# Optimization experiments

Measured on AMD Instinct MI355X. Metric: run time of the kernel, lower is better.

Reference implementation:

```python
import jax, jax.numpy as jnp
import numpy as np

B, D, H, W = 32, 64, 32, 32
M = 1024  # codebook_size


def setup_inputs() -> dict:
    key = jax.random.key(0)
    k1, k2, k3 = jax.random.split(key, 3)
    z = jax.random.normal(k1, (B, D, H, W), dtype=jnp.float32)
    codebook = jax.random.normal(k2, (M, D), dtype=jnp.float32)
    noise = jax.random.normal(k3, (B * H * W, D), dtype=jnp.float32)
    return {"z": z, "codebook": codebook, "noise": noise}


def reference(z, codebook, noise):
    b, d, h, w = z.shape
    n = b * h * w
    # (B,D,H,W) -> (B,H,W,D) -> (N,D)
    zf = jnp.transpose(z, (0, 2, 3, 1)).reshape(n, d)
    x2 = jnp.sum(zf * zf, axis=1, keepdims=True)          # (N,1)
    y2 = jnp.sum(codebook * codebook, axis=1)[None, :]    # (1,M)
    dist = x2 + y2 - 2.0 * (zf @ codebook.T)              # (N,M)
    dist_min = jnp.min(dist, axis=1, keepdims=True)       # (N,1)
    ind = jnp.argmin(dist, axis=1)                        # (N,) int
    # noise substitution: unit-norm random direction scaled by sqrt(min dist)
    nrm = jnp.maximum(jnp.linalg.norm(noise, axis=-1, keepdims=True), 1e-9)
    q_error = noise / nrm * jnp.sqrt(jnp.maximum(dist_min, 0.0))
    z_q = zf + q_error                                    # (N,D)
    # torch: z_q.view(B, D, H*W) is a raw memory reshape of the (B*H*W, D) buffer
    z_q_view = z_q.reshape(b, d, h * w)                   # (B,D,HW)
    # loss = mean over (B,HW,HW) of z_q_view^T @ z_q_view
    #      = sum_b sum_d (sum_n z_q_view[b,d,n])^2 / (B * HW^2)  (no HWxHW intermediate)
    s = jnp.sum(z_q_view, axis=2)                         # (B,D)
    hw = h * w
    loss = jnp.sum(s * s) / (b * hw * hw)
    z_q_out = jnp.transpose(z_q.reshape(b, h, w, d), (0, 3, 1, 2))  # (B,D,H,W)
    return z_q_out, loss, ind
```

## Files before the change

kernel.cpp:

```cpp
#include <hip/hip_runtime.h>
#include <hip/hip_bf16.h>

#define BB 32
#define DD 64
#define HW 1024
#define NN 32768
#define MM 1024

typedef _Float16 half8 __attribute__((ext_vector_type(8)));
typedef float    floatx4 __attribute__((ext_vector_type(4)));

#define MFMA16(a, b, c) __builtin_amdgcn_mfma_f32_16x16x32_f16((a), (b), (c), 0, 0, 0)

#define LO_SCALE   2048.0f
#define LO_INV     (1.0f / 2048.0f)

typedef __attribute__((address_space(1))) const void* gas_t;
typedef __attribute__((address_space(3)))       void* las_t;
#define ASYNC16(g, l) __builtin_amdgcn_global_load_lds((gas_t)(g), (las_t)(l), 16, 0, 0)

__global__ void k_prep(const float* __restrict__ cb,
                       _Float16* __restrict__ ch,
                       _Float16* __restrict__ cl,
                       float* __restrict__ y2,
                       float* __restrict__ loss_slot) {
    int u = blockIdx.x * blockDim.x + threadIdx.x;
    if (u == 0) *loss_slot = 0.0f;

    if (u < 64 * 2 * 64) {
        int lane  = u & 63;
        int kstep = (u >> 6) & 1;
        int mtile = u >> 7;
        int m  = mtile * 16 + (lane & 15);
        int d0 = kstep * 32 + ((lane >> 4) & 3) * 8;
        const float* src = cb + (size_t)m * DD + d0;
        half8 h, l;
#pragma unroll
        for (int j = 0; j < 8; ++j) {
            float x = -2.0f * src[j];
            _Float16 hi = (_Float16)x;
            _Float16 lo = (_Float16)((x - (float)hi) * LO_SCALE);
            h[j] = hi;
            l[j] = lo;
        }
        *(half8*)(ch + (size_t)u * 8) = h;
        *(half8*)(cl + (size_t)u * 8) = l;
    }

    if (u < MM) {
        const float4* c4 = (const float4*)(cb + (size_t)u * DD);
        float s = 0.f;
#pragma unroll
        for (int k = 0; k < 16; ++k) {
            float4 v = c4[k];
            s += v.x * v.x + v.y * v.y + v.z * v.z + v.w * v.w;
        }
        y2[u] = s;
    }
}

__global__ __launch_bounds__(512) void k_main(const float* __restrict__ z,
                                              const float* __restrict__ noise,
                                              const _Float16* __restrict__ ch,
                                              const _Float16* __restrict__ cl,
                                              const float* __restrict__ y2,
                                              float* __restrict__ zq,
                                              float* __restrict__ ind_out,
                                              float* __restrict__ loss_slot) {
    __shared__ float zt[64][65];
    __shared__ float y2s[MM];
    __shared__ float x2p[64][8];
    __shared__ float snorm[64];
    __shared__ float scale_s[64];
    __shared__ float bestv_s[4][64];
    __shared__ int   besti_s[4][64];
    __shared__ float partials[512];
    __shared__ float sq[4];
    __shared__ __align__(16) char ubuf[2 * 16384];

    half8* bufB8 = (half8*)ubuf;
    float (*nt)[65] = (float (*)[65])ubuf;

    const int t    = threadIdx.x;
    const int lane = t & 63;
    const int wv   = t >> 6;
    const int mi   = wv & 3;
    const int rh   = wv >> 2;
    const int quad = lane >> 4;
    const int col  = lane & 15;
    const int blk  = blockIdx.x;
    const int b    = blk >> 4;
    const int hw0  = (blk & 15) << 6;

    const half8* ch8 = (const half8*)ch;
    const half8* cl8 = (const half8*)cl;

    const half8* gseg = (wv < 4) ? (ch8 + wv * 128) : (cl8 + (wv - 4) * 128);
    half8* l0 = bufB8 + wv * 128;
    half8* l1 = bufB8 + 1024 + wv * 128;

    ASYNC16(gseg + lane,      l0);
    ASYNC16(gseg + 64 + lane, l0 + 64);

    const float* zbase = z + ((size_t)b << 16) + hw0;

    for (int i = t; i < 64 * 64; i += 512) {
        int d = i >> 6, r = i & 63;
        zt[r][d] = zbase[(size_t)d * HW + r];
    }
    for (int i = t; i < MM; i += 512) y2s[i] = y2[i];
    __syncthreads();

    {
        int row = t & 63, seg = t >> 6;
        float s = 0.f;
#pragma unroll
        for (int j = 0; j < 8; ++j) {
            float v = zt[row][seg * 8 + j];
            s = __builtin_fmaf(v, v, s);
        }
        x2p[row][seg] = s;
    }

    half8 ah[2][2], al[2][2];
#pragma unroll
    for (int n2 = 0; n2 < 2; ++n2) {
        int row = rh * 32 + n2 * 16 + col;
#pragma unroll
        for (int ks = 0; ks < 2; ++ks) {
            int d0 = ks * 32 + quad * 8;
            half8 h, l;
#pragma unroll
            for (int j = 0; j < 8; ++j) {
                float x = zt[row][d0 + j];
                _Float16 hi = (_Float16)x;
                _Float16 lo = (_Float16)((x - (float)hi) * LO_SCALE);
                h[j] = hi;
                l[j] = lo;
            }
            ah[n2][ks] = h;
            al[n2][ks] = l;
        }
    }

    float best[8];
    int   bmt[8];
#pragma unroll
    for (int s = 0; s < 8; ++s) { best[s] = 1e30f; bmt[s] = 0; }

#pragma unroll 2
    for (int c = 0; c < 16; ++c) {
        const int p = c & 1;
        if (c) __syncthreads();

        if (c < 15) {
            const half8* gs = gseg + (c + 1) * 512;
            half8* ls = ((c + 1) & 1) ? l1 : l0;
            ASYNC16(gs + lane,      ls);
            ASYNC16(gs + 64 + lane, ls + 64);
        }

        const half8* bp = bufB8 + p * 1024;
        half8 bh0 = bp[(mi * 2 + 0) * 64 + lane];
        half8 bh1 = bp[(mi * 2 + 1) * 64 + lane];
        half8 bl0 = bp[512 + (mi * 2 + 0) * 64 + lane];
        half8 bl1 = bp[512 + (mi * 2 + 1) * 64 + lane];

        const int mt = c * 4 + mi;
        float y2v = y2s[(mt << 4) + col];
        floatx4 a1[2], a2[2];
#pragma unroll
        for (int n2 = 0; n2 < 2; ++n2) {
            floatx4 i1 = {y2v, y2v, y2v, y2v};
            floatx4 i2 = {0.f, 0.f, 0.f, 0.f};
            a1[n2] = i1;
            a2[n2] = i2;
        }
#pragma unroll
        for (int n2 = 0; n2 < 2; ++n2) {
            a1[n2] = MFMA16(ah[n2][0], bh0, a1[n2]);
            a2[n2] = MFMA16(al[n2][0], bh0, a2[n2]);
            a2[n2] = MFMA16(ah[n2][0], bl0, a2[n2]);
            a1[n2] = MFMA16(ah[n2][1], bh1, a1[n2]);
            a2[n2] = MFMA16(al[n2][1], bh1, a2[n2]);
            a2[n2] = MFMA16(ah[n2][1], bl1, a2[n2]);
        }
#pragma unroll
        for (int n2 = 0; n2 < 2; ++n2) {
#pragma unroll
            for (int r = 0; r < 4; ++r) {
                float v = __builtin_fmaf(a2[n2][r], LO_INV, a1[n2][r]);
                int s = n2 * 4 + r;
                bool cc = v < best[s];
                best[s] = cc ? v : best[s];
                bmt[s]  = cc ? mt : bmt[s];
            }
        }
    }
    __syncthreads();

    {
        const float4* noise4 = (const float4*)noise;
        const size_t base4 = (size_t)blk * 1024;
#pragma unroll
        for (int k = 0; k < 2; ++k) {
            int v = t + 512 * k;
            float4 vv = noise4[base4 + v];
            int c  = v >> 4;
            int d0 = (v & 15) << 2;
            nt[d0 + 0][c] = vv.x;
            nt[d0 + 1][c] = vv.y;
            nt[d0 + 2][c] = vv.z;
            nt[d0 + 3][c] = vv.w;
            float p = vv.x * vv.x + vv.y * vv.y + vv.z * vv.z + vv.w * vv.w;
            p += __shfl_xor(p, 1);
            p += __shfl_xor(p, 2);
            p += __shfl_xor(p, 4);
            p += __shfl_xor(p, 8);
            if ((t & 15) == 0) snorm[c] = p;
        }
    }

#pragma unroll
    for (int n2 = 0; n2 < 2; ++n2) {
#pragma unroll
        for (int r = 0; r < 4; ++r) {
            int s = n2 * 4 + r;
            float v  = best[s];
            int  idx = bmt[s] * 16 + col;
#pragma unroll
            for (int mask = 1; mask <= 8; mask <<= 1) {
                float v2 = __shfl_xor(v, mask);
                int   i2 = __shfl_xor(idx, mask);
                if (v2 < v || (v2 == v && i2 < idx)) { v = v2; idx = i2; }
            }
            if (col == 0) {
                int rl = rh * 32 + n2 * 16 + quad * 4 + r;
                bestv_s[mi][rl] = v;
                besti_s[mi][rl] = idx;
            }
        }
    }
    __syncthreads();

    if (t < 64) {
        float bv = bestv_s[0][t];
        int   bi = besti_s[0][t];
#pragma unroll
        for (int w = 1; w < 4; ++w) {
            float v = bestv_s[w][t];
            int   ix = besti_s[w][t];
            if (v < bv || (v == bv && ix < bi)) { bv = v; bi = ix; }
        }
        float x2 = 0.f;
#pragma unroll
        for (int s = 0; s < 8; ++s) x2 += x2p[t][s];
        float dm = x2 + bv;
        int n = (blk << 6) + t;
        ind_out[n] = (float)bi;
        float nr = fmaxf(sqrtf(snorm[t]), 1e-9f);
        scale_s[t] = sqrtf(fmaxf(dm, 0.f)) / nr;
    }
    __syncthreads();

    float acc = 0.f;
    const size_t obase = ((size_t)b << 16) + hw0;
#pragma unroll
    for (int it = 0; it < 8; ++it) {
        int flat = it * 512 + t;
        int d = flat >> 6;
        int c = t & 63;
        float v = zt[c][d] + nt[d][c] * scale_s[c];
        zq[obase + (size_t)d * HW + c] = v;
        acc += v;
    }

    partials[t] = acc;
    __syncthreads();
    if (t < 4) {
        float s = 0.f;
        for (int g = 0; g < 8; ++g)
            for (int j = 0; j < 16; ++j)
                s += partials[g * 64 + t * 16 + j];
        sq[t] = s * s;
    }
    __syncthreads();
    if (t == 0) {
        float contrib = (sq[0] + sq[1] + sq[2] + sq[3]) * (1.0f / 33554432.0f);
        atomicAdd(loss_slot, contrib);
    }
}

extern "C" void kernel_launch(void* const* d_in, const int* in_sizes, int n_in,
                              void* d_out, int out_size, void* d_ws, size_t ws_size,
                              hipStream_t stream) {
    const float* z        = (const float*)d_in[0];
    const float* codebook = (const float*)d_in[1];
    const float* noise    = (const float*)d_in[2];

    float* out      = (float*)d_out;
    float* zq_out   = out;
    float* loss_ptr = out + 2097152;
    float* ind_out  = out + 2097153;

    float* y2       = (float*)d_ws;
    _Float16* ch    = (_Float16*)(y2 + MM);
    _Float16* cl    = ch + 65536;

    k_prep<<<16,  512, 0, stream>>>(codebook, ch, cl, y2, loss_ptr);
    k_main<<<512, 512, 0, stream>>>(z, noise, ch, cl, y2,
                                    zq_out, ind_out, loss_ptr);
}
```

Before: 99.95 us.

## Double rows per block to 128 and halve grid to reuse codebook tiles

Each block now handles 128 spatial rows instead of 64, with 8 waves arranged as 4 row groups by 2 codebook groups, each wave covering two 16-wide codebook tiles per chunk. This halves the number of blocks and so halves total codebook streaming through LDS per output row, amortizing the async codebook loads over more MFMA work. Noise staging, the reductions and the loss partials are resized to match. The trade-off is 256 blocks on a GPU with 256 CUs, so there is less parallelism to hide latency, plus higher LDS use per block.

```diff
diff --git a/kernel.cpp b/kernel.cpp
--- a/kernel.cpp
+++ b/kernel.cpp
@@ -67,30 +67,30 @@
                                               float* __restrict__ zq,
                                               float* __restrict__ ind_out,
                                               float* __restrict__ loss_slot) {
-    __shared__ float zt[64][65];
+    __shared__ float zt[128][65];
     __shared__ float y2s[MM];
-    __shared__ float x2p[64][8];
-    __shared__ float snorm[64];
-    __shared__ float scale_s[64];
-    __shared__ float bestv_s[4][64];
-    __shared__ int   besti_s[4][64];
+    __shared__ float x2p[128][4];
+    __shared__ float snorm[128];
+    __shared__ float scale_s[128];
+    __shared__ float bestv_s[2][128];
+    __shared__ int   besti_s[2][128];
     __shared__ float partials[512];
-    __shared__ float sq[4];
-    __shared__ __align__(16) char ubuf[2 * 16384];
+    __shared__ float sq[8];
+    __shared__ __align__(16) char ubuf[33024];
 
     half8* bufB8 = (half8*)ubuf;
-    float (*nt)[65] = (float (*)[65])ubuf;
+    float (*nt)[129] = (float (*)[129])ubuf;
 
     const int t    = threadIdx.x;
     const int lane = t & 63;
     const int wv   = t >> 6;
-    const int mi   = wv & 3;
-    const int rh   = wv >> 2;
+    const int mi   = wv & 1;
+    const int rh   = wv >> 1;
     const int quad = lane >> 4;
     const int col  = lane & 15;
     const int blk  = blockIdx.x;
-    const int b    = blk >> 4;
-    const int hw0  = (blk & 15) << 6;
+    const int b    = blk >> 3;
+    const int hw0  = (blk & 7) << 7;
 
     const half8* ch8 = (const half8*)ch;
     const half8* cl8 = (const half8*)cl;
@@ -104,19 +104,19 @@
 
     const float* zbase = z + ((size_t)b << 16) + hw0;
 
-    for (int i = t; i < 64 * 64; i += 512) {
-        int d = i >> 6, r = i & 63;
+    for (int i = t; i < 128 * 64; i += 512) {
+        int d = i >> 7, r = i & 127;
         zt[r][d] = zbase[(size_t)d * HW + r];
     }
     for (int i = t; i < MM; i += 512) y2s[i] = y2[i];
     __syncthreads();
 
     {
-        int row = t & 63, seg = t >> 6;
+        int row = t & 127, seg = t >> 7;
         float s = 0.f;
 #pragma unroll
-        for (int j = 0; j < 8; ++j) {
-            float v = zt[row][seg * 8 + j];
+        for (int j = 0; j < 16; ++j) {
+            float v = zt[row][seg * 16 + j];
             s = __builtin_fmaf(v, v, s);
         }
         x2p[row][seg] = s;
@@ -161,39 +161,44 @@
         }
 
         const half8* bp = bufB8 + p * 1024;
-        half8 bh0 = bp[(mi * 2 + 0) * 64 + lane];
-        half8 bh1 = bp[(mi * 2 + 1) * 64 + lane];
-        half8 bl0 = bp[512 + (mi * 2 + 0) * 64 + lane];
-        half8 bl1 = bp[512 + (mi * 2 + 1) * 64 + lane];
-
-        const int mt = c * 4 + mi;
-        float y2v = y2s[(mt << 4) + col];
-        floatx4 a1[2], a2[2];
-#pragma unroll
-        for (int n2 = 0; n2 < 2; ++n2) {
-            floatx4 i1 = {y2v, y2v, y2v, y2v};
-            floatx4 i2 = {0.f, 0.f, 0.f, 0.f};
-            a1[n2] = i1;
-            a2[n2] = i2;
-        }
-#pragma unroll
-        for (int n2 = 0; n2 < 2; ++n2) {
-            a1[n2] = MFMA16(ah[n2][0], bh0, a1[n2]);
-            a2[n2] = MFMA16(al[n2][0], bh0, a2[n2]);
-            a2[n2] = MFMA16(ah[n2][0], bl0, a2[n2]);
-            a1[n2] = MFMA16(ah[n2][1], bh1, a1[n2]);
-            a2[n2] = MFMA16(al[n2][1], bh1, a2[n2]);
-            a2[n2] = MFMA16(ah[n2][1], bl1, a2[n2]);
-        }
-#pragma unroll
-        for (int n2 = 0; n2 < 2; ++n2) {
-#pragma unroll
-            for (int r = 0; r < 4; ++r) {
-                float v = __builtin_fmaf(a2[n2][r], LO_INV, a1[n2][r]);
-                int s = n2 * 4 + r;
-                bool cc = v < best[s];
-                best[s] = cc ? v : best[s];
-                bmt[s]  = cc ? mt : bmt[s];
+
+#pragma unroll
+        for (int m2 = 0; m2 < 2; ++m2) {
+            const int ml = mi * 2 + m2;
+            half8 bh0 = bp[(ml * 2 + 0) * 64 + lane];
+            half8 bh1 = bp[(ml * 2 + 1) * 64 + lane];
+            half8 bl0 = bp[512 + (ml * 2 + 0) * 64 + lane];
+            half8 bl1 = bp[512 + (ml * 2 + 1) * 64 + lane];
+
+            const int mt = c * 4 + ml;
+            float y2v = y2s[(mt << 4) + col];
+            floatx4 a1[2], a2[2];
+#pragma unroll
+            for (int n2 = 0; n2 < 2; ++n2) {
+                floatx4 i1 = {y2v, y2v, y2v, y2v};
+                floatx4 i2 = {0.f, 0.f, 0.f, 0.f};
+                a1[n2] = i1;
+                a2[n2] = i2;
+            }
+#pragma unroll
+            for (int n2 = 0; n2 < 2; ++n2) {
+                a1[n2] = MFMA16(ah[n2][0], bh0, a1[n2]);
+                a2[n2] = MFMA16(al[n2][0], bh0, a2[n2]);
+                a2[n2] = MFMA16(ah[n2][0], bl0, a2[n2]);
+                a1[n2] = MFMA16(ah[n2][1], bh1, a1[n2]);
+                a2[n2] = MFMA16(al[n2][1], bh1, a2[n2]);
+                a2[n2] = MFMA16(ah[n2][1], bl1, a2[n2]);
+            }
+#pragma unroll
+            for (int n2 = 0; n2 < 2; ++n2) {
+#pragma unroll
+                for (int r = 0; r < 4; ++r) {
+                    float v = __builtin_fmaf(a2[n2][r], LO_INV, a1[n2][r]);
+                    int s = n2 * 4 + r;
+                    bool cc = v < best[s];
+                    best[s] = cc ? v : best[s];
+                    bmt[s]  = cc ? mt : bmt[s];
+                }
             }
         }
     }
@@ -201,9 +206,9 @@
 
     {
         const float4* noise4 = (const float4*)noise;
-        const size_t base4 = (size_t)blk * 1024;
-#pragma unroll
-        for (int k = 0; k < 2; ++k) {
+        const size_t base4 = (size_t)blk * 2048;
+#pragma unroll
+        for (int k = 0; k < 4; ++k) {
             int v = t + 512 * k;
             float4 vv = noise4[base4 + v];
             int c  = v >> 4;
@@ -243,20 +248,17 @@
     }
     __syncthreads();
 
-    if (t < 64) {
+    if (t < 128) {
         float bv = bestv_s[0][t];
         int   bi = besti_s[0][t];
-#pragma unroll
-        for (int w = 1; w < 4; ++w) {
-            float v = bestv_s[w][t];
-            int   ix = besti_s[w][t];
+        {
+            float v = bestv_s[1][t];
+            int   ix = besti_s[1][t];
             if (v < bv || (v == bv && ix < bi)) { bv = v; bi = ix; }
         }
-        float x2 = 0.f;
-#pragma unroll
-        for (int s = 0; s < 8; ++s) x2 += x2p[t][s];
+        float x2 = x2p[t][0] + x2p[t][1] + x2p[t][2] + x2p[t][3];
         float dm = x2 + bv;
-        int n = (blk << 6) + t;
+        int n = (blk << 7) + t;
         ind_out[n] = (float)bi;
         float nr = fmaxf(sqrtf(snorm[t]), 1e-9f);
         scale_s[t] = sqrtf(fmaxf(dm, 0.f)) / nr;
@@ -266,10 +268,10 @@
     float acc = 0.f;
     const size_t obase = ((size_t)b << 16) + hw0;
 #pragma unroll
-    for (int it = 0; it < 8; ++it) {
+    for (int it = 0; it < 16; ++it) {
         int flat = it * 512 + t;
-        int d = flat >> 6;
-        int c = t & 63;
+        int d = flat >> 7;
+        int c = flat & 127;
         float v = zt[c][d] + nt[d][c] * scale_s[c];
         zq[obase + (size_t)d * HW + c] = v;
         acc += v;
@@ -277,17 +279,19 @@
 
     partials[t] = acc;
     __syncthreads();
-    if (t < 4) {
+    if (t < 8) {
         float s = 0.f;
-        for (int g = 0; g < 8; ++g)
+        for (int cp = 0; cp < 4; ++cp)
             for (int j = 0; j < 16; ++j)
-                s += partials[g * 64 + t * 16 + j];
+                s += partials[cp * 128 + t * 16 + j];
         sq[t] = s * s;
     }
     __syncthreads();
     if (t == 0) {
-        float contrib = (sq[0] + sq[1] + sq[2] + sq[3]) * (1.0f / 33554432.0f);
-        atomicAdd(loss_slot, contrib);
+        float c8 = 0.f;
+#pragma unroll
+        for (int g = 0; g < 8; ++g) c8 += sq[g];
+        atomicAdd(loss_slot, c8 * (1.0f / 33554432.0f));
     }
 }
 
@@ -308,6 +312,6 @@
     _Float16* cl    = ch + 65536;
 
     k_prep<<<16,  512, 0, stream>>>(codebook, ch, cl, y2, loss_ptr);
-    k_main<<<512, 512, 0, stream>>>(z, noise, ch, cl, y2,
+    k_main<<<256, 512, 0, stream>>>(z, noise, ch, cl, y2,
                                     zq_out, ind_out, loss_ptr);
 }
```

New measurement: 103.0 us. 1.03x slower.
